# Kernel tuning notes

Measured on AMD Instinct MI355X. Metric: run time of the kernel, lower is better.

## Reference

```python
import jax, jax.numpy as jnp
import numpy as np

PAD_VAL = -999
N_TYPES = 8
D_IN, D_FF, D_FFC = 512, 1024, 512
B, S = 64, 512


def setup_inputs() -> dict:
    key = jax.random.key(0)
    ks = jax.random.split(key, 6)
    sc = 0.02
    return {
        "x": jax.random.normal(ks[0], (B, S, D_IN), dtype=jnp.float32),
        "sc_types": jax.random.randint(ks[1], (B, S), 0, N_TYPES, dtype=jnp.int64),
        "W_pre": jax.random.normal(ks[2], (D_IN, D_FF), dtype=jnp.float32) * sc,
        "W_types": jax.random.normal(ks[3], (N_TYPES, D_FF, D_IN), dtype=jnp.float32) * sc,
        "W_c1": jax.random.normal(ks[4], (D_IN, D_FFC), dtype=jnp.float32) * sc,
        "W_c2": jax.random.normal(ks[5], (D_FFC, 1), dtype=jnp.float32) * sc,
    }


def reference(x, sc_types, W_pre, W_types, W_c1, W_c2):
    # flatten tokens: [B*S, d_in], [B*S]
    x = x.reshape(-1, x.shape[-1])
    t = sc_types.reshape(-1)
    # (inputs contain no PAD_VAL tokens, so the pad mask is all-True and the
    # gather x[mask] is the identity; shapes stay static)
    x_ = jax.nn.relu(x @ W_pre)                       # [N, d_ff]
    # hard type routing: select per-type MLP output for each token
    x_types = jnp.zeros_like(x)
    for i in range(N_TYPES):
        yi = jax.nn.relu(x_ @ W_types[i])             # [N, d_in]
        x_types = jnp.where((t == i)[:, None], yi, x_types)
    x = x + x_types                                    # residual combine
    h = jax.nn.relu(x @ W_c1)                          # [N, d_ffc]
    return h @ W_c2                                    # [N, 1]
```

## Files before the change

### kernel.cpp

```cpp
#include <hip/hip_runtime.h>
#include <stdint.h>

#define N_TOK 32768
#define DIN   512
#define DFF   1024
#define MPAD  33792

__device__ __forceinline__ int rotk(int k, int row) {
    return (k & ~127) + (((k & 127) + ((row & 15) << 3)) & 127);
}

typedef __attribute__((ext_vector_type(8))) short bf16x8;
typedef __attribute__((ext_vector_type(4))) float f32x4;

__device__ __forceinline__ unsigned short f2bf(float f) {
    union { float f; unsigned int u; } v; v.f = f;
    unsigned int u = v.u;
    return (unsigned short)((u + 0x7FFFu + ((u >> 16) & 1u)) >> 16);
}
__device__ __forceinline__ float bf2f(unsigned int bits) {
    union { unsigned int u; float f; } v; v.u = bits << 16; return v.f;
}
__device__ __forceinline__ unsigned int pk4_fp8(float a, float b, float c, float d) {
    int v = __builtin_amdgcn_cvt_pk_fp8_f32(a, b, 0, false);
    v = __builtin_amdgcn_cvt_pk_fp8_f32(c, d, v, true);
    return (unsigned int)v;
}
__device__ __forceinline__ unsigned char f2fp8(float a) {
    return (unsigned char)(__builtin_amdgcn_cvt_pk_fp8_f32(a, a, 0, false) & 0xFF);
}

__device__ __forceinline__ void async16(const void* g, void* l) {
    __builtin_amdgcn_global_load_lds(
        (const __attribute__((address_space(1))) void*)g,
        (__attribute__((address_space(3))) void*)l, 16, 0, 0);
}

__global__ void prep_kernel(const float* __restrict__ x,
                            unsigned short* __restrict__ Xb,
                            unsigned char* __restrict__ Xb8,
                            const int* __restrict__ types,
                            int* __restrict__ blockhist,
                            const float* __restrict__ Wp,
                            const float* __restrict__ Wt,
                            const float* __restrict__ Wc,
                            unsigned char* __restrict__ Wp8,
                            unsigned char* __restrict__ Wt8,
                            unsigned short* __restrict__ WcT,
                            int* __restrict__ perm) {
    __shared__ float tile[32][33];
    __shared__ int lc[8];
    const int b = blockIdx.x, tid = threadIdx.x;
    if (b < 16384) {
        const int i = b * 1024 + tid * 4;
        float4 v = *(const float4*)(x + i);
        ushort4 o;
        o.x = f2bf(v.x); o.y = f2bf(v.y); o.z = f2bf(v.z); o.w = f2bf(v.w);
        *(ushort4*)(Xb + i) = o;
        const int row = i >> 9;
        const int k   = i & 511;
        *(unsigned int*)(Xb8 + (size_t)row * DIN + rotk(k, row)) = pk4_fp8(v.x, v.y, v.z, v.w);
        if (b < 64) {
            if (tid < 8) lc[tid] = 0;
            __syncthreads();
            atomicAdd(&lc[types[b * 512 + tid]], 1);
            atomicAdd(&lc[types[b * 512 + 256 + tid]], 1);
            __syncthreads();
            if (tid < 8) blockhist[b * 8 + tid] = lc[tid];
        }
    } else if (b < 26624) {
        const int r = b - 16384;
        const int z = r >> 10;
        const int bx = r & 31, by = (r >> 5) & 31;
        const int tx = tid & 31, ty = tid >> 5;
        const float* s; int K, N;
        if (z == 0)      { s = Wp;                          K = 512;  N = 1024; }
        else if (z <= 8) { s = Wt + (size_t)(z-1)*DIN*DFF;  K = 1024; N = 512; }
        else             { s = Wc;                          K = 512;  N = 512; }
        const int n0 = bx * 32, k0 = by * 32;
        if (n0 >= N || k0 >= K) return;
        for (int i = ty; i < 32; i += 8)
            tile[i][tx] = s[(size_t)(k0 + i) * N + n0 + tx];
        __syncthreads();
        if (z == 0) {
            for (int i = ty; i < 32; i += 8) {
                int n = n0 + i;
                Wp8[(size_t)n * K + rotk(k0 + tx, n)] = f2fp8(tile[tx][i] * 64.f);
            }
        } else if (z <= 8) {
            unsigned char* d = Wt8 + (size_t)(z-1)*DIN*DFF;
            for (int i = ty; i < 32; i += 8) {
                int n = n0 + i;
                d[(size_t)n * K + rotk(k0 + tx, n)] = f2fp8(tile[tx][i] * 64.f);
            }
        } else {
            for (int i = ty; i < 32; i += 8)
                WcT[(size_t)(n0 + i) * K + k0 + tx] = f2bf(tile[tx][i]);
        }
    } else {
        perm[(b - 26624) * 256 + tid] = -1;
    }
}

__global__ void scatter_kernel(const int* __restrict__ types,
                               const int* __restrict__ blockhist,
                               int* __restrict__ perm,
                               int* __restrict__ invperm,
                               float* __restrict__ outz,
                               int* __restrict__ po_out) {
    __shared__ int tots[8], base[8], fill[8];
    const int blk = blockIdx.x;
    const int tid = threadIdx.x;
    const int i = blk * 512 + tid;
    outz[i] = 0.f;
    int pre = 0;
    if (tid < 8) {
        int total = 0;
        for (int j = 0; j < 64; j++) {
            int v = blockhist[j * 8 + tid];
            if (j < blk) pre += v;
            total += v;
        }
        tots[tid] = total;
    }
    __syncthreads();
    if (tid < 8) {
        int off = 0, pob = 0;
        #pragma unroll
        for (int t2 = 0; t2 < 8; t2++) {
            if (t2 == tid) pob = off;
            off += ((tots[t2] + 127) >> 7) << 7;
        }
        base[tid] = pob + pre;
        fill[tid] = 0;
        if (blk == 0) {
            po_out[tid] = pob;
            if (tid == 0) po_out[8] = off;
        }
    }
    __syncthreads();
    const int t = types[i];
    const int r = atomicAdd(&fill[t], 1);
    const int p = base[t] + r;
    perm[p] = i;
    invperm[i] = p;
}

template <int MODE>
__global__ __launch_bounds__(256, 4)
void gemm_fp8_kernel(const unsigned char* __restrict__ A,
                     const unsigned char* __restrict__ B,
                     void* __restrict__ Cout,
                     const unsigned short* __restrict__ xres,
                     const int* __restrict__ pmap,
                     const int* __restrict__ po,
                     int K, int ldA) {
    __shared__ unsigned char As[128 * 128];
    __shared__ unsigned char Bs[128 * 128];
    __shared__ int ptile[128];

    const int tid  = threadIdx.x;
    const int wave = tid >> 6;
    const int lane = tid & 63;
    const int quad = lane >> 4;
    const int tl   = lane & 15;
    const int m0 = blockIdx.y * 128;
    const int n0 = blockIdx.x * 128;
    const int wm = (wave & 1) * 64;
    const int wn = (wave >> 1) * 64;

    const unsigned char* Bp = B;
    if constexpr (MODE == 1) {
        if (m0 >= po[8]) return;
        int bsel = 0;
        #pragma unroll
        for (int i = 1; i < 8; i++) bsel += (m0 >= po[i]) ? 1 : 0;
        Bp = B + (size_t)bsel * (DIN * DFF);
    }
    if (tid < 128) ptile[tid] = pmap[m0 + tid];

    f32x4 acc[4][4];
    #pragma unroll
    for (int i = 0; i < 4; i++)
        #pragma unroll
        for (int j = 0; j < 4; j++)
            acc[i][j] = (f32x4){0.f, 0.f, 0.f, 0.f};

    for (int k0 = 0; k0 < K; k0 += 128) {
        __syncthreads();
        #pragma unroll
        for (int i = 0; i < 4; i++) {
            const int c   = (i * 4 + wave) * 64 + lane;
            const int row = c >> 3;
            const int j   = c & 7;
            async16(A + (size_t)(m0 + row) * ldA + k0 + j * 16, (char*)As + (size_t)c * 16);
        }
        #pragma unroll
        for (int i = 0; i < 4; i++) {
            const int c   = (i * 4 + wave) * 64 + lane;
            const int row = c >> 3;
            const int j   = c & 7;
            async16(Bp + (size_t)(n0 + row) * K + k0 + j * 16, (char*)Bs + (size_t)c * 16);
        }
        __syncthreads();

        #pragma unroll
        for (int ks = 0; ks < 4; ks++) {
            long af[4], bfr[4];
            const int o = (ks * 32 + quad * 8 + tl * 8) & 127;
            #pragma unroll
            for (int t = 0; t < 4; t++)
                af[t] = *(const long*)(As + (wm + t * 16 + tl) * 128 + o);
            #pragma unroll
            for (int t = 0; t < 4; t++)
                bfr[t] = *(const long*)(Bs + (wn + t * 16 + tl) * 128 + o);
            #pragma unroll
            for (int mt = 0; mt < 4; mt++)
                #pragma unroll
                for (int nt = 0; nt < 4; nt++)
                    acc[mt][nt] = __builtin_amdgcn_mfma_f32_16x16x32_fp8_fp8(
                        bfr[nt], af[mt], acc[mt][nt], 0, 0, 0);
        }
    }

    if constexpr (MODE == 0) {
        unsigned char* C8 = (unsigned char*)Cout;
        #pragma unroll
        for (int mt = 0; mt < 4; mt++) {
            const int p = ptile[wm + mt * 16 + tl];
            const size_t rowbase = (size_t)p * DFF;
            const int prot = (p & 15) << 3;
            #pragma unroll
            for (int nt = 0; nt < 4; nt++) {
                const int off = wn + nt * 16 + quad * 4;
                unsigned int pk = pk4_fp8(fmaxf(acc[mt][nt][0], 0.f) * 0.125f,
                                          fmaxf(acc[mt][nt][1], 0.f) * 0.125f,
                                          fmaxf(acc[mt][nt][2], 0.f) * 0.125f,
                                          fmaxf(acc[mt][nt][3], 0.f) * 0.125f);
                const int phys = (off & ~127) + (((off & 127) + prot) & 127);
                *(unsigned int*)(C8 + rowbase + n0 + phys) = pk;
            }
        }
    } else {
        unsigned short* Cb = (unsigned short*)Cout;
        #pragma unroll
        for (int mt = 0; mt < 4; mt++) {
            int tok = ptile[wm + mt * 16 + tl];
            if (tok < 0) continue;
            const size_t rowbase = (size_t)tok * DIN;
            #pragma unroll
            for (int nt = 0; nt < 4; nt++) {
                const int ncol = n0 + wn + nt * 16 + quad * 4;
                ushort4 rv = *(const ushort4*)(xres + rowbase + ncol);
                ushort4 o;
                o.x = f2bf(bf2f(rv.x) + fmaxf(acc[mt][nt][0], 0.f) * 0.001953125f);
                o.y = f2bf(bf2f(rv.y) + fmaxf(acc[mt][nt][1], 0.f) * 0.001953125f);
                o.z = f2bf(bf2f(rv.z) + fmaxf(acc[mt][nt][2], 0.f) * 0.001953125f);
                o.w = f2bf(bf2f(rv.w) + fmaxf(acc[mt][nt][3], 0.f) * 0.001953125f);
                *(ushort4*)(Cb + rowbase + ncol) = o;
            }
        }
    }
}

__global__ __launch_bounds__(512, 4)
void gemm3_kernel(const unsigned short* __restrict__ A,
                  const unsigned short* __restrict__ B,
                  const float* __restrict__ w2,
                  float* __restrict__ outp,
                  int K, int ldA) {
    __shared__ unsigned short As[128 * 64];
    __shared__ unsigned short Bs[256 * 64];

    const int tid  = threadIdx.x;
    const int wave = tid >> 6;
    const int lane = tid & 63;
    const int quad = lane >> 4;
    const int tl   = lane & 15;
    const int m0 = blockIdx.y * 128;
    const int n0 = blockIdx.x * 256;
    const int wm = (wave & 1) * 64;
    const int wn = (wave >> 1) * 64;

    f32x4 acc[4][4];
    #pragma unroll
    for (int i = 0; i < 4; i++)
        #pragma unroll
        for (int j = 0; j < 4; j++)
            acc[i][j] = (f32x4){0.f, 0.f, 0.f, 0.f};

    for (int k0 = 0; k0 < K; k0 += 64) {
        __syncthreads();
        #pragma unroll
        for (int i = 0; i < 2; i++) {
            const int c   = (i * 8 + wave) * 64 + lane;
            const int row = c >> 3;
            const int gj  = (c & 7) ^ (row & 7);
            async16(A + (size_t)(m0 + row) * ldA + k0 + gj * 8, (char*)As + (size_t)c * 16);
        }
        #pragma unroll
        for (int i = 0; i < 4; i++) {
            const int c   = (i * 8 + wave) * 64 + lane;
            const int row = c >> 3;
            const int gj  = (c & 7) ^ (row & 7);
            async16(B + (size_t)(n0 + row) * K + k0 + gj * 8, (char*)Bs + (size_t)c * 16);
        }
        __syncthreads();

        #pragma unroll
        for (int ks = 0; ks < 2; ks++) {
            bf16x8 af[4], bfr[4];
            const int jc = ks * 4 + quad;
            #pragma unroll
            for (int t = 0; t < 4; t++) {
                const int r = wm + t * 16 + tl;
                af[t] = *(const bf16x8*)(As + (r * 8 + (jc ^ (r & 7))) * 8);
            }
            #pragma unroll
            for (int t = 0; t < 4; t++) {
                const int r = wn + t * 16 + tl;
                bfr[t] = *(const bf16x8*)(Bs + (r * 8 + (jc ^ (r & 7))) * 8);
            }
            #pragma unroll
            for (int mt = 0; mt < 4; mt++)
                #pragma unroll
                for (int nt = 0; nt < 4; nt++)
                    acc[mt][nt] = __builtin_amdgcn_mfma_f32_16x16x32_bf16(
                        bfr[nt], af[mt], acc[mt][nt], 0, 0, 0);
        }
    }

    float4 w2v[4];
    #pragma unroll
    for (int nt = 0; nt < 4; nt++)
        w2v[nt] = *(const float4*)(w2 + n0 + wn + nt * 16 + quad * 4);
    #pragma unroll
    for (int mt = 0; mt < 4; mt++) {
        float s = 0.f;
        #pragma unroll
        for (int nt = 0; nt < 4; nt++) {
            s += fmaxf(acc[mt][nt][0], 0.f) * w2v[nt].x;
            s += fmaxf(acc[mt][nt][1], 0.f) * w2v[nt].y;
            s += fmaxf(acc[mt][nt][2], 0.f) * w2v[nt].z;
            s += fmaxf(acc[mt][nt][3], 0.f) * w2v[nt].w;
        }
        s += __shfl_down(s, 32);
        s += __shfl_down(s, 16);
        if (lane < 16) atomicAdd(&outp[m0 + wm + mt * 16 + lane], s);
    }
}

extern "C" void kernel_launch(void* const* d_in, const int* in_sizes, int n_in,
                              void* d_out, int out_size, void* d_ws, size_t ws_size,
                              hipStream_t stream) {
    const float* x      = (const float*)d_in[0];
    const int*   types  = (const int*)d_in[1];
    const float* W_pre  = (const float*)d_in[2];
    const float* W_types= (const float*)d_in[3];
    const float* W_c1   = (const float*)d_in[4];
    const float* W_c2   = (const float*)d_in[5];
    float* out = (float*)d_out;

    char* ws = (char*)d_ws;
    unsigned short* Xb  = (unsigned short*)(ws);
    unsigned char*  Xff8= (unsigned char*)(ws + 33554432ull);
    unsigned char*  Xb8 = (unsigned char*)(ws + 68157440ull);
    unsigned char*  Wp8 = (unsigned char*)(ws + 84934656ull);
    unsigned char*  Wt8 = (unsigned char*)(ws + 85458944ull);
    unsigned short* WcT = (unsigned short*)(ws + 89653248ull);
    int* perm           = (int*)(ws + 90177536ull);
    int* invperm        = (int*)(ws + 90312704ull);
    int* po             = (int*)(ws + 90443776ull);
    int* blockhist      = po + 16;

    prep_kernel<<<26756, 256, 0, stream>>>(x, Xb, Xb8, types, blockhist,
                                           W_pre, W_types, W_c1, Wp8, Wt8, WcT, perm);
    scatter_kernel<<<64, 512, 0, stream>>>(types, blockhist, perm, invperm, out, po);
    gemm_fp8_kernel<0><<<dim3(DFF / 128, N_TOK / 128), 256, 0, stream>>>(
        Xb8, Wp8, Xff8, nullptr, invperm, nullptr, 512, 512);
    gemm_fp8_kernel<1><<<dim3(DIN / 128, MPAD / 128), 256, 0, stream>>>(
        Xff8, Wt8, Xb, Xb, perm, po, 1024, 1024);
    gemm3_kernel<<<dim3(DIN / 256, N_TOK / 128), 512, 0, stream>>>(
        Xb, WcT, W_c2, out, 512, 512);
}
```

Before: 231.6 us.

## Add 256x256 double-buffered 8-phase FP8 kernel for first GEMM

Replaces the generic 128x128 FP8 GEMM for the W_pre projection with a dedicated 512-thread kernel using 256x256 tiles. Global-to-LDS async loads for the next K slice are double-buffered and interleaved across eight compute phases, with MFMA sections raised in wave priority. Block IDs are remapped to an XCD-aware order. This aims to raise data reuse per tile and hide load latency behind compute. In exchange it uses 128KB of LDS per block and more accumulator registers, which lowers occupancy.

```diff
diff --git a/kernel.cpp b/kernel.cpp
--- a/kernel.cpp
+++ b/kernel.cpp
@@ -146,6 +146,123 @@
     invperm[i] = p;
 }
 
+__global__ __launch_bounds__(512, 2)
+void gemm1_fp8_8ph(const unsigned char* __restrict__ A,
+                   const unsigned char* __restrict__ B,
+                   unsigned char* __restrict__ C8,
+                   const int* __restrict__ invperm) {
+    __shared__ unsigned char As[2][256 * 128];
+    __shared__ unsigned char Bs[2][256 * 128];
+    __shared__ int ptile[256];
+
+    const int tid  = threadIdx.x;
+    const int wave = tid >> 6;
+    const int lane = tid & 63;
+    const int quad = lane >> 4;
+    const int tl   = lane & 15;
+
+    const int lin  = blockIdx.x;
+    const int sid  = (lin & 7) * 64 + (lin >> 3);
+    const int m0   = (sid >> 2) * 256;
+    const int n0   = (sid & 3) * 256;
+
+    const int wm = (wave & 1) * 128;
+    const int wn = (wave >> 1) * 64;
+
+    if (tid < 256) ptile[tid] = invperm[m0 + tid];
+
+    f32x4 acc[8][4];
+    #pragma unroll
+    for (int i = 0; i < 8; i++)
+        #pragma unroll
+        for (int j = 0; j < 4; j++)
+            acc[i][j] = (f32x4){0.f, 0.f, 0.f, 0.f};
+
+    #pragma unroll
+    for (int ci = 0; ci < 8; ++ci) {
+        const int c = ci * 512 + tid;
+        if (ci < 4) {
+            const int row = c >> 3, j = c & 7;
+            async16(A + (size_t)(m0 + row) * 512 + j * 16, &As[0][c * 16]);
+        } else {
+            const int c2 = c - 2048;
+            const int row = c2 >> 3, j = c2 & 7;
+            async16(B + (size_t)(n0 + row) * 512 + j * 16, &Bs[0][c2 * 16]);
+        }
+    }
+    asm volatile("s_waitcnt vmcnt(0)" ::: "memory");
+    __builtin_amdgcn_s_barrier();
+    asm volatile("" ::: "memory");
+
+    for (int t = 0; t < 4; ++t) {
+        const unsigned char* Asl = As[t & 1];
+        const unsigned char* Bsl = Bs[t & 1];
+        unsigned char* Asn = As[(t + 1) & 1];
+        unsigned char* Bsn = Bs[(t + 1) & 1];
+        const int k0n = (t + 1) * 128;
+        const bool st = (t < 3);
+        #pragma unroll
+        for (int ph = 0; ph < 8; ++ph) {
+            const int ks = ph >> 1, mh = ph & 1;
+            const int o = (ks * 32 + quad * 8 + tl * 8) & 127;
+            long af[4], bfr[4];
+            #pragma unroll
+            for (int mt = 0; mt < 4; ++mt)
+                af[mt] = *(const long*)(Asl + (wm + mh * 64 + mt * 16 + tl) * 128 + o);
+            #pragma unroll
+            for (int nt = 0; nt < 4; ++nt)
+                bfr[nt] = *(const long*)(Bsl + (wn + nt * 16 + tl) * 128 + o);
+            if (st && ph < 4) {
+                #pragma unroll
+                for (int u = 0; u < 2; ++u) {
+                    const int cidx = ph * 2 + u;
+                    const int c = cidx * 512 + tid;
+                    if (cidx < 4) {
+                        const int row = c >> 3, j = c & 7;
+                        async16(A + (size_t)(m0 + row) * 512 + k0n + j * 16, Asn + c * 16);
+                    } else {
+                        const int c2 = c - 2048;
+                        const int row = c2 >> 3, j = c2 & 7;
+                        async16(B + (size_t)(n0 + row) * 512 + k0n + j * 16, Bsn + c2 * 16);
+                    }
+                }
+            }
+            __builtin_amdgcn_s_barrier();
+            asm volatile("" ::: "memory");
+            __builtin_amdgcn_s_setprio(1);
+            #pragma unroll
+            for (int mt = 0; mt < 4; ++mt)
+                #pragma unroll
+                for (int nt = 0; nt < 4; ++nt)
+                    acc[mh * 4 + mt][nt] = __builtin_amdgcn_mfma_f32_16x16x32_fp8_fp8(
+                        bfr[nt], af[mt], acc[mh * 4 + mt][nt], 0, 0, 0);
+            __builtin_amdgcn_s_setprio(0);
+            if (ph == 7) asm volatile("s_waitcnt vmcnt(0)" ::: "memory");
+            __builtin_amdgcn_s_barrier();
+            asm volatile("" ::: "memory");
+        }
+    }
+
+    #pragma unroll
+    for (int mh = 0; mh < 2; ++mh)
+        #pragma unroll
+        for (int mt = 0; mt < 4; ++mt) {
+            const int p = ptile[wm + mh * 64 + mt * 16 + tl];
+            const size_t rowbase = (size_t)p * DFF;
+            const int prot = (p & 15) << 3;
+            #pragma unroll
+            for (int nt = 0; nt < 4; ++nt) {
+                const int off = wn + nt * 16 + quad * 4;
+                unsigned int pk = pk4_fp8(fmaxf(acc[mh * 4 + mt][nt][0], 0.f) * 0.125f,
+                                          fmaxf(acc[mh * 4 + mt][nt][1], 0.f) * 0.125f,
+                                          fmaxf(acc[mh * 4 + mt][nt][2], 0.f) * 0.125f,
+                                          fmaxf(acc[mh * 4 + mt][nt][3], 0.f) * 0.125f);
+                const int phys = (off & ~127) + (((off & 127) + prot) & 127);
+                *(unsigned int*)(C8 + rowbase + n0 + phys) = pk;
+            }
+        }
+}
+
 template <int MODE>
 __global__ __launch_bounds__(256, 4)
 void gemm_fp8_kernel(const unsigned char* __restrict__ A,
@@ -376,8 +493,7 @@
     prep_kernel<<<26756, 256, 0, stream>>>(x, Xb, Xb8, types, blockhist,
                                            W_pre, W_types, W_c1, Wp8, Wt8, WcT, perm);
     scatter_kernel<<<64, 512, 0, stream>>>(types, blockhist, perm, invperm, out, po);
-    gemm_fp8_kernel<0><<<dim3(DFF / 128, N_TOK / 128), 256, 0, stream>>>(
-        Xb8, Wp8, Xff8, nullptr, invperm, nullptr, 512, 512);
+    gemm1_fp8_8ph<<<512, 512, 0, stream>>>(Xb8, Wp8, Xff8, invperm);
     gemm_fp8_kernel<1><<<dim3(DIN / 128, MPAD / 128), 256, 0, stream>>>(
         Xff8, Wt8, Xb, Xb, perm, po, 1024, 1024);
     gemm3_kernel<<<dim3(DIN / 256, N_TOK / 128), 512, 0, stream>>>(
```

After: 232.8 us. No clear change (+0.5%).

## Use 1024-thread fp8 GEMM blocks, XCD-aware tile remap, vectorized weight packing

Applied to the files above, without the earlier changes.

The fp8 GEMMs move from 256 threads with 4x4 MFMA tiles per wave to 1024 threads with 2x2 tiles per wave, so each thread issues one async load per operand per k-step. Block indices are remapped so consecutive tiles stay on the same XCD, which should improve L2 reuse, and the same remap is applied to gemm3. The weight conversion writes four packed fp8 values per store instead of single bytes, and the residual epilogue loads its inputs before doing the math. Smaller per-wave tiles reduce register use but cut MFMA reuse from LDS and add synchronization across 16 waves.

```diff
diff --git a/kernel.cpp b/kernel.cpp
--- a/kernel.cpp
+++ b/kernel.cpp
@@ -82,17 +82,15 @@
         for (int i = ty; i < 32; i += 8)
             tile[i][tx] = s[(size_t)(k0 + i) * N + n0 + tx];
         __syncthreads();
-        if (z == 0) {
-            for (int i = ty; i < 32; i += 8) {
-                int n = n0 + i;
-                Wp8[(size_t)n * K + rotk(k0 + tx, n)] = f2fp8(tile[tx][i] * 64.f);
-            }
-        } else if (z <= 8) {
-            unsigned char* d = Wt8 + (size_t)(z-1)*DIN*DFF;
-            for (int i = ty; i < 32; i += 8) {
-                int n = n0 + i;
-                d[(size_t)n * K + rotk(k0 + tx, n)] = f2fp8(tile[tx][i] * 64.f);
-            }
+        if (z <= 8) {
+            unsigned char* d = (z == 0) ? Wp8 : (Wt8 + (size_t)(z-1)*DIN*DFF);
+            const int nl = tid >> 3;
+            const int k4 = (tid & 7) << 2;
+            const int n  = n0 + nl;
+            const int kk = k0 + k4;
+            unsigned int pk = pk4_fp8(tile[k4 + 0][nl] * 64.f, tile[k4 + 1][nl] * 64.f,
+                                      tile[k4 + 2][nl] * 64.f, tile[k4 + 3][nl] * 64.f);
+            *(unsigned int*)(d + (size_t)n * K + rotk(kk, n)) = pk;
         } else {
             for (int i = ty; i < 32; i += 8)
                 WcT[(size_t)(n0 + i) * K + k0 + tx] = f2bf(tile[tx][i]);
@@ -147,7 +145,7 @@
 }
 
 template <int MODE>
-__global__ __launch_bounds__(256, 4)
+__global__ __launch_bounds__(1024, 8)
 void gemm_fp8_kernel(const unsigned char* __restrict__ A,
                      const unsigned char* __restrict__ B,
                      void* __restrict__ Cout,
@@ -164,10 +162,18 @@
     const int lane = tid & 63;
     const int quad = lane >> 4;
     const int tl   = lane & 15;
-    const int m0 = blockIdx.y * 128;
-    const int n0 = blockIdx.x * 128;
-    const int wm = (wave & 1) * 64;
-    const int wn = (wave >> 1) * 64;
+    int m0, n0;
+    if constexpr (MODE == 1) {
+        const int sid = (blockIdx.x & 7) * 132 + (blockIdx.x >> 3);
+        m0 = (sid >> 2) * 128;
+        n0 = (sid & 3) * 128;
+    } else {
+        const int sid = (blockIdx.x & 7) * 256 + (blockIdx.x >> 3);
+        m0 = (sid >> 3) * 128;
+        n0 = (sid & 7) * 128;
+    }
+    const int wm = (wave >> 2) * 32;
+    const int wn = (wave & 3) * 32;
 
     const unsigned char* Bp = B;
     if constexpr (MODE == 1) {
@@ -179,45 +185,38 @@
     }
     if (tid < 128) ptile[tid] = pmap[m0 + tid];
 
-    f32x4 acc[4][4];
+    f32x4 acc[2][2];
     #pragma unroll
-    for (int i = 0; i < 4; i++)
-        #pragma unroll
-        for (int j = 0; j < 4; j++)
+    for (int i = 0; i < 2; i++)
+        #pragma unroll
+        for (int j = 0; j < 2; j++)
             acc[i][j] = (f32x4){0.f, 0.f, 0.f, 0.f};
 
+    const int arow = tid >> 3;
+    const int aj   = (tid & 7) * 16;
+    const unsigned char* aptr = A + (size_t)(m0 + arow) * ldA + aj;
+    const unsigned char* bptr = Bp + (size_t)(n0 + arow) * K + aj;
+
     for (int k0 = 0; k0 < K; k0 += 128) {
         __syncthreads();
-        #pragma unroll
-        for (int i = 0; i < 4; i++) {
-            const int c   = (i * 4 + wave) * 64 + lane;
-            const int row = c >> 3;
-            const int j   = c & 7;
-            async16(A + (size_t)(m0 + row) * ldA + k0 + j * 16, (char*)As + (size_t)c * 16);
-        }
-        #pragma unroll
-        for (int i = 0; i < 4; i++) {
-            const int c   = (i * 4 + wave) * 64 + lane;
-            const int row = c >> 3;
-            const int j   = c & 7;
-            async16(Bp + (size_t)(n0 + row) * K + k0 + j * 16, (char*)Bs + (size_t)c * 16);
-        }
+        async16(aptr + k0, (char*)As + tid * 16);
+        async16(bptr + k0, (char*)Bs + tid * 16);
         __syncthreads();
 
         #pragma unroll
         for (int ks = 0; ks < 4; ks++) {
-            long af[4], bfr[4];
+            long af[2], bfr[2];
             const int o = (ks * 32 + quad * 8 + tl * 8) & 127;
             #pragma unroll
-            for (int t = 0; t < 4; t++)
+            for (int t = 0; t < 2; t++)
                 af[t] = *(const long*)(As + (wm + t * 16 + tl) * 128 + o);
             #pragma unroll
-            for (int t = 0; t < 4; t++)
+            for (int t = 0; t < 2; t++)
                 bfr[t] = *(const long*)(Bs + (wn + t * 16 + tl) * 128 + o);
             #pragma unroll
-            for (int mt = 0; mt < 4; mt++)
+            for (int mt = 0; mt < 2; mt++)
                 #pragma unroll
-                for (int nt = 0; nt < 4; nt++)
+                for (int nt = 0; nt < 2; nt++)
                     acc[mt][nt] = __builtin_amdgcn_mfma_f32_16x16x32_fp8_fp8(
                         bfr[nt], af[mt], acc[mt][nt], 0, 0, 0);
         }
@@ -226,12 +225,12 @@
     if constexpr (MODE == 0) {
         unsigned char* C8 = (unsigned char*)Cout;
         #pragma unroll
-        for (int mt = 0; mt < 4; mt++) {
+        for (int mt = 0; mt < 2; mt++) {
             const int p = ptile[wm + mt * 16 + tl];
             const size_t rowbase = (size_t)p * DFF;
             const int prot = (p & 15) << 3;
             #pragma unroll
-            for (int nt = 0; nt < 4; nt++) {
+            for (int nt = 0; nt < 2; nt++) {
                 const int off = wn + nt * 16 + quad * 4;
                 unsigned int pk = pk4_fp8(fmaxf(acc[mt][nt][0], 0.f) * 0.125f,
                                           fmaxf(acc[mt][nt][1], 0.f) * 0.125f,
@@ -243,20 +242,30 @@
         }
     } else {
         unsigned short* Cb = (unsigned short*)Cout;
-        #pragma unroll
-        for (int mt = 0; mt < 4; mt++) {
-            int tok = ptile[wm + mt * 16 + tl];
-            if (tok < 0) continue;
-            const size_t rowbase = (size_t)tok * DIN;
-            #pragma unroll
-            for (int nt = 0; nt < 4; nt++) {
+        int toks[2];
+        #pragma unroll
+        for (int mt = 0; mt < 2; mt++) toks[mt] = ptile[wm + mt * 16 + tl];
+        ushort4 rv[2][2];
+        #pragma unroll
+        for (int mt = 0; mt < 2; mt++) {
+            if (toks[mt] < 0) continue;
+            const size_t rowbase = (size_t)toks[mt] * DIN;
+            #pragma unroll
+            for (int nt = 0; nt < 2; nt++)
+                rv[mt][nt] = *(const ushort4*)(xres + rowbase + n0 + wn + nt * 16 + quad * 4);
+        }
+        #pragma unroll
+        for (int mt = 0; mt < 2; mt++) {
+            if (toks[mt] < 0) continue;
+            const size_t rowbase = (size_t)toks[mt] * DIN;
+            #pragma unroll
+            for (int nt = 0; nt < 2; nt++) {
                 const int ncol = n0 + wn + nt * 16 + quad * 4;
-                ushort4 rv = *(const ushort4*)(xres + rowbase + ncol);
                 ushort4 o;
-                o.x = f2bf(bf2f(rv.x) + fmaxf(acc[mt][nt][0], 0.f) * 0.001953125f);
-                o.y = f2bf(bf2f(rv.y) + fmaxf(acc[mt][nt][1], 0.f) * 0.001953125f);
-                o.z = f2bf(bf2f(rv.z) + fmaxf(acc[mt][nt][2], 0.f) * 0.001953125f);
-                o.w = f2bf(bf2f(rv.w) + fmaxf(acc[mt][nt][3], 0.f) * 0.001953125f);
+                o.x = f2bf(bf2f(rv[mt][nt].x) + fmaxf(acc[mt][nt][0], 0.f) * 0.001953125f);
+                o.y = f2bf(bf2f(rv[mt][nt].y) + fmaxf(acc[mt][nt][1], 0.f) * 0.001953125f);
+                o.z = f2bf(bf2f(rv[mt][nt].z) + fmaxf(acc[mt][nt][2], 0.f) * 0.001953125f);
+                o.w = f2bf(bf2f(rv[mt][nt].w) + fmaxf(acc[mt][nt][3], 0.f) * 0.001953125f);
                 *(ushort4*)(Cb + rowbase + ncol) = o;
             }
         }
@@ -277,8 +286,9 @@
     const int lane = tid & 63;
     const int quad = lane >> 4;
     const int tl   = lane & 15;
-    const int m0 = blockIdx.y * 128;
-    const int n0 = blockIdx.x * 256;
+    const int sid = (blockIdx.x & 7) * 64 + (blockIdx.x >> 3);
+    const int m0 = (sid >> 1) * 128;
+    const int n0 = (sid & 1) * 256;
     const int wm = (wave & 1) * 64;
     const int wn = (wave >> 1) * 64;
 
@@ -376,10 +386,10 @@
     prep_kernel<<<26756, 256, 0, stream>>>(x, Xb, Xb8, types, blockhist,
                                            W_pre, W_types, W_c1, Wp8, Wt8, WcT, perm);
     scatter_kernel<<<64, 512, 0, stream>>>(types, blockhist, perm, invperm, out, po);
-    gemm_fp8_kernel<0><<<dim3(DFF / 128, N_TOK / 128), 256, 0, stream>>>(
+    gemm_fp8_kernel<0><<<2048, 1024, 0, stream>>>(
         Xb8, Wp8, Xff8, nullptr, invperm, nullptr, 512, 512);
-    gemm_fp8_kernel<1><<<dim3(DIN / 128, MPAD / 128), 256, 0, stream>>>(
+    gemm_fp8_kernel<1><<<1056, 1024, 0, stream>>>(
         Xff8, Wt8, Xb, Xb, perm, po, 1024, 1024);
-    gemm3_kernel<<<dim3(DIN / 256, N_TOK / 128), 512, 0, stream>>>(
+    gemm3_kernel<<<512, 512, 0, stream>>>(
         Xb, WcT, W_c2, out, 512, 512);
 }
```

Result: no change. 233.7 us (+0.9%).
